# Performance work log

Measured on AMD Instinct MI355X. Metric: run time of the kernel, lower is better.

The kernel has to match this reference:

```python
import jax, jax.numpy as jnp
import numpy as np

LOW_DIM, SKIP_DIM, OUT_DIM = 512, 256, 256
EPS_IDW = 1e-8
EPS_LN = 1e-5
K = 3


def setup_inputs() -> dict:
    key = jax.random.key(0)
    ks = jax.random.split(key, 10)
    B, N, S = 4, 8192, 2048
    xyz_hi = jax.random.uniform(ks[0], (B, N, 3), dtype=jnp.float32)
    xyz_lo = jax.random.uniform(ks[1], (B, S, 3), dtype=jnp.float32)
    feat_skip = jax.random.normal(ks[2], (B, N, SKIP_DIM), dtype=jnp.float32)
    feat_lo = jax.random.normal(ks[3], (B, S, LOW_DIM), dtype=jnp.float32)
    in_dim = LOW_DIM + SKIP_DIM
    W1 = jax.random.normal(ks[4], (in_dim, OUT_DIM), dtype=jnp.float32) / np.sqrt(in_dim)
    b1 = jnp.zeros((OUT_DIM,), dtype=jnp.float32)
    W2 = jax.random.normal(ks[5], (OUT_DIM, OUT_DIM), dtype=jnp.float32) / np.sqrt(OUT_DIM)
    b2 = jnp.zeros((OUT_DIM,), dtype=jnp.float32)
    gamma = jnp.ones((OUT_DIM,), dtype=jnp.float32)
    beta = jnp.zeros((OUT_DIM,), dtype=jnp.float32)
    return {"xyz_hi": xyz_hi, "xyz_lo": xyz_lo, "feat_skip": feat_skip,
            "feat_lo": feat_lo, "W1": W1, "b1": b1, "W2": W2, "b2": b2,
            "gamma": gamma, "beta": beta}


def _layer_norm(x, gamma, beta):
    mu = jnp.mean(x, axis=-1, keepdims=True)
    var = jnp.mean(jnp.square(x - mu), axis=-1, keepdims=True)
    return (x - mu) * jax.lax.rsqrt(var + EPS_LN) * gamma + beta


def reference(xyz_hi, xyz_lo, feat_skip, feat_lo, W1, b1, W2, b2, gamma, beta):
    B, N, _ = xyz_hi.shape
    _, S, _ = xyz_lo.shape
    if S == 1:
        interpolated = jnp.broadcast_to(feat_lo, (B, N, feat_lo.shape[-1]))
    else:
        # pairwise Euclidean distances: (B, N, S)
        d2 = (jnp.sum(xyz_hi ** 2, -1)[:, :, None]
              + jnp.sum(xyz_lo ** 2, -1)[:, None, :]
              - 2.0 * jnp.einsum('bnd,bsd->bns', xyz_hi, xyz_lo))
        dists = jnp.sqrt(jnp.maximum(d2, 0.0))
        # smallest-3 via top_k on negated distances
        neg_d, knn_idx = jax.lax.top_k(-dists, K)          # (B, N, 3)
        dk = -neg_d
        inv_d = 1.0 / (dk + EPS_IDW)
        weights = inv_d / jnp.sum(inv_d, axis=-1, keepdims=True)  # (B, N, 3)
        # gather neighbor features: (B, N, 3, low_dim)
        knn_feat = feat_lo[jnp.arange(B)[:, None, None], knn_idx]
        interpolated = jnp.einsum('bnk,bnkc->bnc', weights, knn_feat)
    fused = jnp.concatenate([feat_skip, interpolated], axis=-1)   # (B, N, skip+low)
    h = jax.nn.relu(fused @ W1 + b1)
    h = h @ W2 + b2
    return _layer_norm(h, gamma, beta)
```

## Files before the change

### kernel.cpp

```cpp
#include <hip/hip_runtime.h>
#include <hip/hip_bf16.h>
#include <stdint.h>

typedef unsigned short u16;
typedef __attribute__((ext_vector_type(8))) short short8;
typedef __attribute__((ext_vector_type(4))) float f32x4;

#define BB 4
#define NN 8192
#define SS 2048
#define MTOT 32768
#define CSKIP 256
#define CLO 512
#define CIN 768
#define COUT 256

__device__ __forceinline__ u16 f2bf(float f) {
  unsigned u = __float_as_uint(f);
  u += 0x7fffu + ((u >> 16) & 1u);
  return (u16)(u >> 16);
}

__device__ __forceinline__ void gl_lds16(const void* g, void* l) {
  __builtin_amdgcn_global_load_lds(
      (const __attribute__((address_space(1))) void*)g,
      (__attribute__((address_space(3))) void*)l, 16, 0, 0);
}

__global__ __launch_bounds__(256) void wconv_kernel(const float* __restrict__ W1,
                                                    const float* __restrict__ W2,
                                                    u16* __restrict__ W1T,
                                                    u16* __restrict__ W2T) {
  int i = blockIdx.x * 256 + threadIdx.x;
  if (i < CIN * COUT) {
    int n = i / CIN, k = i - n * CIN;
    W1T[i] = f2bf(W1[(size_t)k * COUT + n]);
  } else if (i < CIN * COUT + COUT * COUT) {
    int j = i - CIN * COUT;
    int n = j >> 8, k = j & 255;
    W2T[j] = f2bf(W2[(size_t)k * COUT + n]);
  }
}

__global__ __launch_bounds__(512) void knn_kernel(
    const float* __restrict__ xyz_hi, const float* __restrict__ xyz_lo,
    float* __restrict__ wq_g, int* __restrict__ iq_g) {
  __shared__ float4 sxyz[SS];
  __shared__ float md[8][64][3];
  __shared__ int   mi[8][64][3];

  int tid = threadIdx.x;
  int blk = blockIdx.x;
  int b = blk >> 7;
  const float* xl = xyz_lo + (size_t)b * SS * 3;
  for (int j = tid; j < SS; j += 512)
    sxyz[j] = make_float4(xl[j * 3 + 0], xl[j * 3 + 1], xl[j * 3 + 2], 0.f);
  __syncthreads();

  int wave = tid >> 6, lane = tid & 63;
  int qm = blk * 64 + lane;
  float qx = xyz_hi[(size_t)qm * 3 + 0];
  float qy = xyz_hi[(size_t)qm * 3 + 1];
  float qz = xyz_hi[(size_t)qm * 3 + 2];

  float b0 = 1e30f, b1 = 1e30f, b2 = 1e30f;
  int i0 = -1, i1 = -1, i2 = -1;
  int j0 = wave * 256;
#pragma unroll 4
  for (int jj = 0; jj < 256; ++jj) {
    int j = j0 + jj;
    float4 p = sxyz[j];
    float dx = p.x - qx, dy = p.y - qy, dz = p.z - qz;
    float d = fmaf(dx, dx, fmaf(dy, dy, dz * dz));
    bool c = d < b2;
    b2 = c ? d : b2; i2 = c ? j : i2;
    bool s = b2 < b1;
    float tb = b1; b1 = s ? b2 : b1; b2 = s ? tb : b2;
    int ti = i1;   i1 = s ? i2 : i1; i2 = s ? ti : i2;
    bool v = b1 < b0;
    float ub = b0; b0 = v ? b1 : b0; b1 = v ? ub : b1;
    int ui = i0;   i0 = v ? i1 : i0; i1 = v ? ui : i1;
  }
  md[wave][lane][0] = b0; mi[wave][lane][0] = i0;
  md[wave][lane][1] = b1; mi[wave][lane][1] = i1;
  md[wave][lane][2] = b2; mi[wave][lane][2] = i2;
  __syncthreads();

  if (tid < 64) {
    int q = tid;
    float fb0 = 1e30f, fb1 = 1e30f, fb2 = 1e30f;
    int fi0 = -1, fi1 = -1, fi2 = -1;
    for (int p = 0; p < 8; ++p)
#pragma unroll
      for (int s = 0; s < 3; ++s) {
        float d = md[p][q][s]; int ix = mi[p][q][s];
        if (d < fb2 || (d == fb2 && ix < fi2)) {
          fb2 = d; fi2 = ix;
          if (fb2 < fb1 || (fb2 == fb1 && fi2 < fi1)) {
            float t = fb1; fb1 = fb2; fb2 = t; int ti = fi1; fi1 = fi2; fi2 = ti;
          }
          if (fb1 < fb0 || (fb1 == fb0 && fi1 < fi0)) {
            float t = fb0; fb0 = fb1; fb1 = t; int ti = fi0; fi0 = fi1; fi1 = ti;
          }
        }
      }
    int qm2 = blk * 64 + q;
    float d0 = sqrtf(fb0), d1 = sqrtf(fb1), d2 = sqrtf(fb2);
    float inv0 = 1.0f / (d0 + 1e-8f);
    float inv1 = 1.0f / (d1 + 1e-8f);
    float inv2 = 1.0f / (d2 + 1e-8f);
    float s = inv0 + inv1 + inv2;
    wq_g[(size_t)qm2 * 3 + 0] = inv0 / s;
    wq_g[(size_t)qm2 * 3 + 1] = inv1 / s;
    wq_g[(size_t)qm2 * 3 + 2] = inv2 / s;
    iq_g[(size_t)qm2 * 3 + 0] = fi0;
    iq_g[(size_t)qm2 * 3 + 1] = fi1;
    iq_g[(size_t)qm2 * 3 + 2] = fi2;
  }
}

__global__ __launch_bounds__(512) void gemm1_fused_kernel(
    const float* __restrict__ feat_skip, const float* __restrict__ feat_lo,
    const float* __restrict__ wq_g, const int* __restrict__ iq_g,
    const u16* __restrict__ W1T, const float* __restrict__ b1,
    u16* __restrict__ H) {
  __shared__ u16 As[128 * 32];
  __shared__ u16 Bs[256 * 32];
  int tid = threadIdx.x;
  int m0 = blockIdx.x << 7;
  int b = blockIdx.x >> 6;
  int w = tid >> 6, lane = tid & 63;
  int wr = w >> 2, wc = w & 3;
  int quad = lane >> 4, l16 = lane & 15;

  int srow = tid >> 2;
  int sc8 = (tid & 3) << 3;
  float w0 = wq_g[(size_t)(m0 + srow) * 3 + 0];
  float w1 = wq_g[(size_t)(m0 + srow) * 3 + 1];
  float w2 = wq_g[(size_t)(m0 + srow) * 3 + 2];
  int i0 = iq_g[(size_t)(m0 + srow) * 3 + 0];
  int i1 = iq_g[(size_t)(m0 + srow) * 3 + 1];
  int i2 = iq_g[(size_t)(m0 + srow) * 3 + 2];
  const float* fl0 = feat_lo + ((size_t)b * SS + i0) * CLO + sc8;
  const float* fl1 = feat_lo + ((size_t)b * SS + i1) * CLO + sc8;
  const float* fl2 = feat_lo + ((size_t)b * SS + i2) * CLO + sc8;
  const float* fsk = feat_skip + (size_t)(m0 + srow) * CSKIP + sc8;
  u16* As_dst = As + srow * 32 + sc8;

  f32x4 zero = {0.f, 0.f, 0.f, 0.f};
  f32x4 acc[4][4];
#pragma unroll
  for (int tm = 0; tm < 4; ++tm)
#pragma unroll
    for (int tn = 0; tn < 4; ++tn) acc[tm][tn] = zero;

  for (int kc = 0; kc < 24; ++kc) {
    __syncthreads();
#pragma unroll
    for (int r = 0; r < 2; ++r) {
      int u = tid + r * 512;
      int nrow = u >> 2, kb = (u & 3) << 3;
      gl_lds16(W1T + (size_t)nrow * CIN + kc * 32 + kb, (char*)Bs + u * 16);
    }
    float av[8];
    if (kc < 8) {
      float4 x0 = *(const float4*)(fsk + kc * 32);
      float4 x1 = *(const float4*)(fsk + kc * 32 + 4);
      av[0] = x0.x; av[1] = x0.y; av[2] = x0.z; av[3] = x0.w;
      av[4] = x1.x; av[5] = x1.y; av[6] = x1.z; av[7] = x1.w;
    } else {
      int c = (kc - 8) * 32;
      float4 a0 = *(const float4*)(fl0 + c), a1 = *(const float4*)(fl0 + c + 4);
      float4 c0 = *(const float4*)(fl1 + c), c1 = *(const float4*)(fl1 + c + 4);
      float4 e0 = *(const float4*)(fl2 + c), e1 = *(const float4*)(fl2 + c + 4);
      av[0] = fmaf(w0, a0.x, fmaf(w1, c0.x, w2 * e0.x));
      av[1] = fmaf(w0, a0.y, fmaf(w1, c0.y, w2 * e0.y));
      av[2] = fmaf(w0, a0.z, fmaf(w1, c0.z, w2 * e0.z));
      av[3] = fmaf(w0, a0.w, fmaf(w1, c0.w, w2 * e0.w));
      av[4] = fmaf(w0, a1.x, fmaf(w1, c1.x, w2 * e1.x));
      av[5] = fmaf(w0, a1.y, fmaf(w1, c1.y, w2 * e1.y));
      av[6] = fmaf(w0, a1.z, fmaf(w1, c1.z, w2 * e1.z));
      av[7] = fmaf(w0, a1.w, fmaf(w1, c1.w, w2 * e1.w));
    }
    union { __hip_bfloat162 h2[4]; uint4 u4; } pk;
#pragma unroll
    for (int c = 0; c < 4; ++c)
      pk.h2[c] = __float22bfloat162_rn(make_float2(av[2 * c], av[2 * c + 1]));
    *(uint4*)As_dst = pk.u4;
    __syncthreads();

    short8 af[4], bf[4];
#pragma unroll
    for (int t = 0; t < 4; ++t)
      af[t] = *(const short8*)(As + ((wr * 64 + t * 16 + l16) * 32 + quad * 8));
#pragma unroll
    for (int t = 0; t < 4; ++t)
      bf[t] = *(const short8*)(Bs + ((wc * 64 + t * 16 + l16) * 32 + quad * 8));
#pragma unroll
    for (int tm = 0; tm < 4; ++tm)
#pragma unroll
      for (int tn = 0; tn < 4; ++tn)
        acc[tm][tn] = __builtin_amdgcn_mfma_f32_16x16x32_bf16(af[tm], bf[tn], acc[tm][tn], 0, 0, 0);
  }

  float bias[4];
#pragma unroll
  for (int tn = 0; tn < 4; ++tn) bias[tn] = b1[wc * 64 + tn * 16 + l16];
#pragma unroll
  for (int tm = 0; tm < 4; ++tm)
#pragma unroll
    for (int tn = 0; tn < 4; ++tn) {
      int col = wc * 64 + tn * 16 + l16;
#pragma unroll
      for (int r = 0; r < 4; ++r) {
        int row = m0 + wr * 64 + tm * 16 + quad * 4 + r;
        float v = acc[tm][tn][r] + bias[tn];
        v = v > 0.f ? v : 0.f;
        H[(size_t)row * COUT + col] = f2bf(v);
      }
    }
}

__global__ __launch_bounds__(512) void gemm2_ln_kernel(const u16* __restrict__ H,
                                                       const u16* __restrict__ Bt,
                                                       const float* __restrict__ b2,
                                                       const float* __restrict__ gamma,
                                                       const float* __restrict__ beta,
                                                       float* __restrict__ out) {
  __shared__ u16 As[128 * 32];
  __shared__ u16 Bs[256 * 32];
  __shared__ float red[4][128][2];
  __shared__ float stats[128][2];
  int tid = threadIdx.x;
  int m0 = blockIdx.x << 7;
  int w = tid >> 6, lane = tid & 63;
  int wr = w >> 2, wc = w & 3;
  int quad = lane >> 4, l16 = lane & 15;

  f32x4 zero = {0.f, 0.f, 0.f, 0.f};
  f32x4 acc[4][4];
#pragma unroll
  for (int tm = 0; tm < 4; ++tm)
#pragma unroll
    for (int tn = 0; tn < 4; ++tn) acc[tm][tn] = zero;

  for (int k0 = 0; k0 < COUT; k0 += 32) {
    __syncthreads();
    {
      int row = tid >> 2, kk = (tid & 3) << 3;
      gl_lds16(H + (size_t)(m0 + row) * COUT + k0 + kk, (char*)As + tid * 16);
#pragma unroll
      for (int r = 0; r < 2; ++r) {
        int ub = tid + r * 512;
        int nrow = ub >> 2, kb = (ub & 3) << 3;
        gl_lds16(Bt + (size_t)nrow * COUT + k0 + kb, (char*)Bs + ub * 16);
      }
    }
    __syncthreads();
    short8 af[4], bf[4];
#pragma unroll
    for (int t = 0; t < 4; ++t)
      af[t] = *(const short8*)(As + ((wr * 64 + t * 16 + l16) * 32 + quad * 8));
#pragma unroll
    for (int t = 0; t < 4; ++t)
      bf[t] = *(const short8*)(Bs + ((wc * 64 + t * 16 + l16) * 32 + quad * 8));
#pragma unroll
    for (int tm = 0; tm < 4; ++tm)
#pragma unroll
      for (int tn = 0; tn < 4; ++tn)
        acc[tm][tn] = __builtin_amdgcn_mfma_f32_16x16x32_bf16(af[tm], bf[tn], acc[tm][tn], 0, 0, 0);
  }

  float bias[4], g[4], be[4];
#pragma unroll
  for (int tn = 0; tn < 4; ++tn) {
    int col = wc * 64 + tn * 16 + l16;
    bias[tn] = b2[col]; g[tn] = gamma[col]; be[tn] = beta[col];
  }
#pragma unroll
  for (int tm = 0; tm < 4; ++tm)
#pragma unroll
    for (int r = 0; r < 4; ++r) {
      float s = 0.f, sq = 0.f;
#pragma unroll
      for (int tn = 0; tn < 4; ++tn) {
        float v = acc[tm][tn][r] + bias[tn];
        acc[tm][tn][r] = v;
        s += v; sq += v * v;
      }
#pragma unroll
      for (int msk = 1; msk < 16; msk <<= 1) {
        s += __shfl_xor(s, msk);
        sq += __shfl_xor(sq, msk);
      }
      if (l16 == 0) {
        int rl = wr * 64 + tm * 16 + quad * 4 + r;
        red[wc][rl][0] = s;
        red[wc][rl][1] = sq;
      }
    }
  __syncthreads();
  if (tid < 128) {
    float s = red[0][tid][0] + red[1][tid][0] + red[2][tid][0] + red[3][tid][0];
    float sq = red[0][tid][1] + red[1][tid][1] + red[2][tid][1] + red[3][tid][1];
    float mu = s * (1.f / 256.f);
    float var = sq * (1.f / 256.f) - mu * mu;
    stats[tid][0] = mu;
    stats[tid][1] = rsqrtf(var + 1e-5f);
  }
  __syncthreads();
#pragma unroll
  for (int tm = 0; tm < 4; ++tm)
#pragma unroll
    for (int r = 0; r < 4; ++r) {
      int rl = wr * 64 + tm * 16 + quad * 4 + r;
      float mu = stats[rl][0], rstd = stats[rl][1];
#pragma unroll
      for (int tn = 0; tn < 4; ++tn) {
        int col = wc * 64 + tn * 16 + l16;
        out[(size_t)(m0 + rl) * COUT + col] = (acc[tm][tn][r] - mu) * rstd * g[tn] + be[tn];
      }
    }
}

extern "C" void kernel_launch(void* const* d_in, const int* in_sizes, int n_in,
                              void* d_out, int out_size, void* d_ws, size_t ws_size,
                              hipStream_t stream) {
  const float* xyz_hi    = (const float*)d_in[0];
  const float* xyz_lo    = (const float*)d_in[1];
  const float* feat_skip = (const float*)d_in[2];
  const float* feat_lo   = (const float*)d_in[3];
  const float* W1        = (const float*)d_in[4];
  const float* b1        = (const float*)d_in[5];
  const float* W2        = (const float*)d_in[6];
  const float* b2        = (const float*)d_in[7];
  const float* gamma     = (const float*)d_in[8];
  const float* beta      = (const float*)d_in[9];
  float* out = (float*)d_out;

  char* ws = (char*)d_ws;
  u16*   H    = (u16*)ws;
  u16*   W1T  = (u16*)(ws + 16777216);
  u16*   W2T  = (u16*)(ws + 16777216 + 393216);
  float* wq_g = (float*)(ws + 16777216 + 393216 + 131072);
  int*   iq_g = (int*)(ws + 16777216 + 393216 + 131072 + 393216);

  wconv_kernel<<<1024, 256, 0, stream>>>(W1, W2, W1T, W2T);
  knn_kernel<<<MTOT / 64, 512, 0, stream>>>(xyz_hi, xyz_lo, wq_g, iq_g);
  gemm1_fused_kernel<<<MTOT / 128, 512, 0, stream>>>(feat_skip, feat_lo, wq_g, iq_g, W1T, b1, H);
  gemm2_ln_kernel<<<MTOT / 128, 512, 0, stream>>>(H, W2T, b2, gamma, beta, out);
}
```

Measured before the change: 197.4 us.

## Double-buffer LDS in both GEMM kernels and shrink row tile to 64

Both GEMM kernels move from 128-row, 512-thread blocks to 64-row, 256-thread blocks and gain double-buffered LDS tiles. The next K-chunk's global loads (B via direct-to-LDS, A gathered into registers) are issued before the current chunk's MFMAs, and one barrier per iteration replaces two. The aim is to hide global load latency behind compute and raise the block count. The cost is twice as many blocks each re-reading the full weight tile, which adds L2 traffic, plus more registers for the prefetched A values.

```diff
diff --git a/kernel.cpp b/kernel.cpp
--- a/kernel.cpp
+++ b/kernel.cpp
@@ -119,18 +119,17 @@
   }
 }
 
-__global__ __launch_bounds__(512) void gemm1_fused_kernel(
+__global__ __launch_bounds__(256) void gemm1_fused_kernel(
     const float* __restrict__ feat_skip, const float* __restrict__ feat_lo,
     const float* __restrict__ wq_g, const int* __restrict__ iq_g,
     const u16* __restrict__ W1T, const float* __restrict__ b1,
     u16* __restrict__ H) {
-  __shared__ u16 As[128 * 32];
-  __shared__ u16 Bs[256 * 32];
+  __shared__ u16 As[2][64 * 32];
+  __shared__ u16 Bs[2][256 * 32];
   int tid = threadIdx.x;
-  int m0 = blockIdx.x << 7;
-  int b = blockIdx.x >> 6;
+  int m0 = blockIdx.x << 6;
+  int b = blockIdx.x >> 7;
   int w = tid >> 6, lane = tid & 63;
-  int wr = w >> 2, wc = w & 3;
   int quad = lane >> 4, l16 = lane & 15;
 
   int srow = tid >> 2;
@@ -145,7 +144,48 @@
   const float* fl1 = feat_lo + ((size_t)b * SS + i1) * CLO + sc8;
   const float* fl2 = feat_lo + ((size_t)b * SS + i2) * CLO + sc8;
   const float* fsk = feat_skip + (size_t)(m0 + srow) * CSKIP + sc8;
-  u16* As_dst = As + srow * 32 + sc8;
+
+  float4 ra[6];
+  auto loadA = [&](int kc) {
+    if (kc < 8) {
+      ra[0] = *(const float4*)(fsk + kc * 32);
+      ra[1] = *(const float4*)(fsk + kc * 32 + 4);
+    } else {
+      int c = (kc - 8) * 32;
+      ra[0] = *(const float4*)(fl0 + c); ra[1] = *(const float4*)(fl0 + c + 4);
+      ra[2] = *(const float4*)(fl1 + c); ra[3] = *(const float4*)(fl1 + c + 4);
+      ra[4] = *(const float4*)(fl2 + c); ra[5] = *(const float4*)(fl2 + c + 4);
+    }
+  };
+  auto packA = [&](int kc, int buf) {
+    float av[8];
+    if (kc < 8) {
+      av[0] = ra[0].x; av[1] = ra[0].y; av[2] = ra[0].z; av[3] = ra[0].w;
+      av[4] = ra[1].x; av[5] = ra[1].y; av[6] = ra[1].z; av[7] = ra[1].w;
+    } else {
+      av[0] = fmaf(w0, ra[0].x, fmaf(w1, ra[2].x, w2 * ra[4].x));
+      av[1] = fmaf(w0, ra[0].y, fmaf(w1, ra[2].y, w2 * ra[4].y));
+      av[2] = fmaf(w0, ra[0].z, fmaf(w1, ra[2].z, w2 * ra[4].z));
+      av[3] = fmaf(w0, ra[0].w, fmaf(w1, ra[2].w, w2 * ra[4].w));
+      av[4] = fmaf(w0, ra[1].x, fmaf(w1, ra[3].x, w2 * ra[5].x));
+      av[5] = fmaf(w0, ra[1].y, fmaf(w1, ra[3].y, w2 * ra[5].y));
+      av[6] = fmaf(w0, ra[1].z, fmaf(w1, ra[3].z, w2 * ra[5].z));
+      av[7] = fmaf(w0, ra[1].w, fmaf(w1, ra[3].w, w2 * ra[5].w));
+    }
+    union { __hip_bfloat162 h2[4]; uint4 u4; } pk;
+#pragma unroll
+    for (int c = 0; c < 4; ++c)
+      pk.h2[c] = __float22bfloat162_rn(make_float2(av[2 * c], av[2 * c + 1]));
+    *(uint4*)(As[buf] + srow * 32 + sc8) = pk.u4;
+  };
+  auto issueB = [&](int kc, int buf) {
+#pragma unroll
+    for (int r = 0; r < 4; ++r) {
+      int u = tid + r * 256;
+      int nrow = u >> 2, kb = (u & 3) << 3;
+      gl_lds16(W1T + (size_t)nrow * CIN + kc * 32 + kb, (char*)Bs[buf] + u * 16);
+    }
+  };
 
   f32x4 zero = {0.f, 0.f, 0.f, 0.f};
   f32x4 acc[4][4];
@@ -154,66 +194,43 @@
 #pragma unroll
     for (int tn = 0; tn < 4; ++tn) acc[tm][tn] = zero;
 
+  loadA(0);
+  issueB(0, 0);
+  packA(0, 0);
+
   for (int kc = 0; kc < 24; ++kc) {
+    int cur = kc & 1, nxt = cur ^ 1;
     __syncthreads();
-#pragma unroll
-    for (int r = 0; r < 2; ++r) {
-      int u = tid + r * 512;
-      int nrow = u >> 2, kb = (u & 3) << 3;
-      gl_lds16(W1T + (size_t)nrow * CIN + kc * 32 + kb, (char*)Bs + u * 16);
-    }
-    float av[8];
-    if (kc < 8) {
-      float4 x0 = *(const float4*)(fsk + kc * 32);
-      float4 x1 = *(const float4*)(fsk + kc * 32 + 4);
-      av[0] = x0.x; av[1] = x0.y; av[2] = x0.z; av[3] = x0.w;
-      av[4] = x1.x; av[5] = x1.y; av[6] = x1.z; av[7] = x1.w;
-    } else {
-      int c = (kc - 8) * 32;
-      float4 a0 = *(const float4*)(fl0 + c), a1 = *(const float4*)(fl0 + c + 4);
-      float4 c0 = *(const float4*)(fl1 + c), c1 = *(const float4*)(fl1 + c + 4);
-      float4 e0 = *(const float4*)(fl2 + c), e1 = *(const float4*)(fl2 + c + 4);
-      av[0] = fmaf(w0, a0.x, fmaf(w1, c0.x, w2 * e0.x));
-      av[1] = fmaf(w0, a0.y, fmaf(w1, c0.y, w2 * e0.y));
-      av[2] = fmaf(w0, a0.z, fmaf(w1, c0.z, w2 * e0.z));
-      av[3] = fmaf(w0, a0.w, fmaf(w1, c0.w, w2 * e0.w));
-      av[4] = fmaf(w0, a1.x, fmaf(w1, c1.x, w2 * e1.x));
-      av[5] = fmaf(w0, a1.y, fmaf(w1, c1.y, w2 * e1.y));
-      av[6] = fmaf(w0, a1.z, fmaf(w1, c1.z, w2 * e1.z));
-      av[7] = fmaf(w0, a1.w, fmaf(w1, c1.w, w2 * e1.w));
-    }
-    union { __hip_bfloat162 h2[4]; uint4 u4; } pk;
-#pragma unroll
-    for (int c = 0; c < 4; ++c)
-      pk.h2[c] = __float22bfloat162_rn(make_float2(av[2 * c], av[2 * c + 1]));
-    *(uint4*)As_dst = pk.u4;
-    __syncthreads();
+    bool more = (kc + 1 < 24);
+    if (more) { loadA(kc + 1); issueB(kc + 1, nxt); }
 
     short8 af[4], bf[4];
 #pragma unroll
     for (int t = 0; t < 4; ++t)
-      af[t] = *(const short8*)(As + ((wr * 64 + t * 16 + l16) * 32 + quad * 8));
+      af[t] = *(const short8*)(As[cur] + ((t * 16 + l16) * 32 + quad * 8));
 #pragma unroll
     for (int t = 0; t < 4; ++t)
-      bf[t] = *(const short8*)(Bs + ((wc * 64 + t * 16 + l16) * 32 + quad * 8));
+      bf[t] = *(const short8*)(Bs[cur] + ((w * 64 + t * 16 + l16) * 32 + quad * 8));
 #pragma unroll
     for (int tm = 0; tm < 4; ++tm)
 #pragma unroll
       for (int tn = 0; tn < 4; ++tn)
         acc[tm][tn] = __builtin_amdgcn_mfma_f32_16x16x32_bf16(af[tm], bf[tn], acc[tm][tn], 0, 0, 0);
+
+    if (more) packA(kc + 1, nxt);
   }
 
   float bias[4];
 #pragma unroll
-  for (int tn = 0; tn < 4; ++tn) bias[tn] = b1[wc * 64 + tn * 16 + l16];
+  for (int tn = 0; tn < 4; ++tn) bias[tn] = b1[w * 64 + tn * 16 + l16];
 #pragma unroll
   for (int tm = 0; tm < 4; ++tm)
 #pragma unroll
     for (int tn = 0; tn < 4; ++tn) {
-      int col = wc * 64 + tn * 16 + l16;
+      int col = w * 64 + tn * 16 + l16;
 #pragma unroll
       for (int r = 0; r < 4; ++r) {
-        int row = m0 + wr * 64 + tm * 16 + quad * 4 + r;
+        int row = m0 + tm * 16 + quad * 4 + r;
         float v = acc[tm][tn][r] + bias[tn];
         v = v > 0.f ? v : 0.f;
         H[(size_t)row * COUT + col] = f2bf(v);
@@ -221,21 +238,32 @@
     }
 }
 
-__global__ __launch_bounds__(512) void gemm2_ln_kernel(const u16* __restrict__ H,
+__global__ __launch_bounds__(256) void gemm2_ln_kernel(const u16* __restrict__ H,
                                                        const u16* __restrict__ Bt,
                                                        const float* __restrict__ b2,
                                                        const float* __restrict__ gamma,
                                                        const float* __restrict__ beta,
                                                        float* __restrict__ out) {
-  __shared__ u16 As[128 * 32];
-  __shared__ u16 Bs[256 * 32];
-  __shared__ float red[4][128][2];
-  __shared__ float stats[128][2];
+  __shared__ u16 As[2][64 * 32];
+  __shared__ u16 Bs[2][256 * 32];
+  __shared__ float red[4][64][2];
+  __shared__ float stats[64][2];
   int tid = threadIdx.x;
-  int m0 = blockIdx.x << 7;
+  int m0 = blockIdx.x << 6;
   int w = tid >> 6, lane = tid & 63;
-  int wr = w >> 2, wc = w & 3;
   int quad = lane >> 4, l16 = lane & 15;
+
+  auto issueAB = [&](int kc, int buf) {
+    int srow = tid >> 2, sc8 = (tid & 3) << 3;
+    gl_lds16(H + (size_t)(m0 + srow) * COUT + kc * 32 + sc8,
+             (char*)As[buf] + tid * 16);
+#pragma unroll
+    for (int r = 0; r < 4; ++r) {
+      int u = tid + r * 256;
+      int nrow = u >> 2, kb = (u & 3) << 3;
+      gl_lds16(Bt + (size_t)nrow * COUT + kc * 32 + kb, (char*)Bs[buf] + u * 16);
+    }
+  };
 
   f32x4 zero = {0.f, 0.f, 0.f, 0.f};
   f32x4 acc[4][4];
@@ -244,26 +272,19 @@
 #pragma unroll
     for (int tn = 0; tn < 4; ++tn) acc[tm][tn] = zero;
 
-  for (int k0 = 0; k0 < COUT; k0 += 32) {
+  issueAB(0, 0);
+  for (int kc = 0; kc < 8; ++kc) {
+    int cur = kc & 1, nxt = cur ^ 1;
     __syncthreads();
-    {
-      int row = tid >> 2, kk = (tid & 3) << 3;
-      gl_lds16(H + (size_t)(m0 + row) * COUT + k0 + kk, (char*)As + tid * 16);
-#pragma unroll
-      for (int r = 0; r < 2; ++r) {
-        int ub = tid + r * 512;
-        int nrow = ub >> 2, kb = (ub & 3) << 3;
-        gl_lds16(Bt + (size_t)nrow * COUT + k0 + kb, (char*)Bs + ub * 16);
-      }
-    }
-    __syncthreads();
+    if (kc + 1 < 8) issueAB(kc + 1, nxt);
+
     short8 af[4], bf[4];
 #pragma unroll
     for (int t = 0; t < 4; ++t)
-      af[t] = *(const short8*)(As + ((wr * 64 + t * 16 + l16) * 32 + quad * 8));
+      af[t] = *(const short8*)(As[cur] + ((t * 16 + l16) * 32 + quad * 8));
 #pragma unroll
     for (int t = 0; t < 4; ++t)
-      bf[t] = *(const short8*)(Bs + ((wc * 64 + t * 16 + l16) * 32 + quad * 8));
+      bf[t] = *(const short8*)(Bs[cur] + ((w * 64 + t * 16 + l16) * 32 + quad * 8));
 #pragma unroll
     for (int tm = 0; tm < 4; ++tm)
 #pragma unroll
@@ -274,7 +295,7 @@
   float bias[4], g[4], be[4];
 #pragma unroll
   for (int tn = 0; tn < 4; ++tn) {
-    int col = wc * 64 + tn * 16 + l16;
+    int col = w * 64 + tn * 16 + l16;
     bias[tn] = b2[col]; g[tn] = gamma[col]; be[tn] = beta[col];
   }
 #pragma unroll
@@ -294,13 +315,13 @@
         sq += __shfl_xor(sq, msk);
       }
       if (l16 == 0) {
-        int rl = wr * 64 + tm * 16 + quad * 4 + r;
-        red[wc][rl][0] = s;
-        red[wc][rl][1] = sq;
+        int rl = tm * 16 + quad * 4 + r;
+        red[w][rl][0] = s;
+        red[w][rl][1] = sq;
       }
     }
   __syncthreads();
-  if (tid < 128) {
+  if (tid < 64) {
     float s = red[0][tid][0] + red[1][tid][0] + red[2][tid][0] + red[3][tid][0];
     float sq = red[0][tid][1] + red[1][tid][1] + red[2][tid][1] + red[3][tid][1];
     float mu = s * (1.f / 256.f);
@@ -313,11 +334,11 @@
   for (int tm = 0; tm < 4; ++tm)
 #pragma unroll
     for (int r = 0; r < 4; ++r) {
-      int rl = wr * 64 + tm * 16 + quad * 4 + r;
+      int rl = tm * 16 + quad * 4 + r;
       float mu = stats[rl][0], rstd = stats[rl][1];
 #pragma unroll
       for (int tn = 0; tn < 4; ++tn) {
-        int col = wc * 64 + tn * 16 + l16;
+        int col = w * 64 + tn * 16 + l16;
         out[(size_t)(m0 + rl) * COUT + col] = (acc[tm][tn][r] - mu) * rstd * g[tn] + be[tn];
       }
     }
@@ -347,6 +368,6 @@
 
   wconv_kernel<<<1024, 256, 0, stream>>>(W1, W2, W1T, W2T);
   knn_kernel<<<MTOT / 64, 512, 0, stream>>>(xyz_hi, xyz_lo, wq_g, iq_g);
-  gemm1_fused_kernel<<<MTOT / 128, 512, 0, stream>>>(feat_skip, feat_lo, wq_g, iq_g, W1T, b1, H);
-  gemm2_ln_kernel<<<MTOT / 128, 512, 0, stream>>>(H, W2T, b2, gamma, beta, out);
-}
+  gemm1_fused_kernel<<<MTOT / 64, 256, 0, stream>>>(feat_skip, feat_lo, wq_g, iq_g, W1T, b1, H);
+  gemm2_ln_kernel<<<MTOT / 64, 256, 0, stream>>>(H, W2T, b2, gamma, beta, out);
+}
```

New measurement: 252.3 us. 27.8% more time.
